# Kernel tuning notes

Hardware: AMD Instinct MI355X
Metric: run time of the kernel (lower is better)

The kernel has to match this reference:

```python
import jax, jax.numpy as jnp
import numpy as np
from jax import lax

B, N, M = 2, 16384, 4096
C1, C2 = 128, 256
H1, H2 = 256, 128  # mlp = [C1+C2, 256, 128]


def setup_inputs() -> dict:
    key = jax.random.key(0)
    ks = jax.random.split(key, 8)
    return {
        "unknown": jax.random.normal(ks[0], (B, N, 3), jnp.float32),
        "known": jax.random.normal(ks[1], (B, M, 3), jnp.float32),
        "unknow_feats": jax.random.normal(ks[2], (B, C1, N), jnp.float32),
        "known_feats": jax.random.normal(ks[3], (B, C2, M), jnp.float32),
        "W1": jax.random.normal(ks[4], (H1, C1 + C2), jnp.float32) * 0.05,
        "b1": jnp.zeros((H1,), jnp.float32),
        "W2": jax.random.normal(ks[5], (H2, H1), jnp.float32) * 0.05,
        "b2": jnp.zeros((H2,), jnp.float32),
    }


def reference(unknown, known, unknow_feats, known_feats, W1, b1, W2, b2):
    # Pairwise squared distances (B, n, m) via ||a||^2 + ||b||^2 - 2 a.b
    d2 = (
        jnp.sum(unknown * unknown, -1)[:, :, None]
        + jnp.sum(known * known, -1)[:, None, :]
        - 2.0 * jnp.einsum("bnd,bmd->bnm", unknown, known)
    )
    # 3 nearest neighbors
    neg_d2, idx = lax.top_k(-d2, 3)  # (B, n, 3)
    dist = jnp.sqrt(jnp.maximum(-neg_d2, 0.0))  # pointops returns sqrt distances
    dist_recip = 1.0 / (dist + 1e-8)
    weight = dist_recip / jnp.sum(dist_recip, axis=2, keepdims=True)  # (B, n, 3)
    # Gather neighbor features (B, C2, n, 3) and inverse-distance weighted sum
    gathered = jax.vmap(lambda f, i: f[:, i])(known_feats, idx)
    interpolated = jnp.sum(gathered * weight[:, None, :, :], axis=-1)  # (B, C2, n)
    new_features = jnp.concatenate([interpolated, unknow_feats], axis=1)  # (B, C1+C2, n)
    # Shared MLP (1x1 convs, bn=False -> conv bias + ReLU)
    h = jax.nn.relu(jnp.einsum("oc,bcn->bon", W1, new_features) + b1[None, :, None])
    out = jax.nn.relu(jnp.einsum("oc,bcn->bon", W2, h) + b2[None, :, None])
    return out  # (B, mlp[-1], n)
```

## Files before the change

kernel.cpp:

```cpp
#include <hip/hip_runtime.h>
#include <hip/hip_bf16.h>

#define BB 2
#define NN 16384
#define MM 4096
#define C1 128
#define C2 256
#define CIN 384
#define H1 256
#define H2 128
#define XROW 392
#define HROW 264
#define OS   36

typedef __attribute__((ext_vector_type(8))) short bf16x8;
typedef __attribute__((ext_vector_type(4))) float f32x4;
typedef __attribute__((ext_vector_type(2))) float f32x2;

__device__ __forceinline__ short f32_to_bf16(float x) {
    unsigned u = __float_as_uint(x);
    u += 0x7fffu + ((u >> 16) & 1u);
    return (short)(u >> 16);
}
__device__ __forceinline__ float bf16_to_f32(unsigned short u) {
    union { unsigned u; float f; } c; c.u = ((unsigned)u) << 16; return c.f;
}
__device__ __forceinline__ unsigned pack_bf16x2(float a, float b) {
    __hip_bfloat162 h = __float22bfloat162_rn(make_float2(a, b));
    union { __hip_bfloat162 h; unsigned u; } cv;
    cv.h = h;
    return cv.u;
}
__device__ __forceinline__ f32x2 score2k(f32x2 ax2, f32x2 ay2, f32x2 az2,
                                         f32x2 kx, f32x2 ky, f32x2 kz, f32x2 kn) {
    f32x2 t = __builtin_elementwise_fma(ay2, ky, kn);
    t = __builtin_elementwise_fma(ax2, kx, t);
    t = __builtin_elementwise_fma(az2, kz, t);
    return t;
}

__global__ __launch_bounds__(256) void prep_kernel(
    const float* __restrict__ KF, unsigned short* __restrict__ KT16,
    const float* __restrict__ W1, const float* __restrict__ W2,
    short* __restrict__ W1b, short* __restrict__ W2b,
    const float* __restrict__ known, float* __restrict__ kxyz)
{
    const int bx  = blockIdx.x;
    const int tid = threadIdx.x;
    if (bx < 512) {
        __shared__ short tlb[64 * 65];
        const int tb = bx >> 8;
        const int c0 = ((bx >> 6) & 3) * 64;
        const int m0 = (bx & 63) * 64;
        const int tr  = tid >> 4;
        const int tc4 = (tid & 15) * 4;
        #pragma unroll
        for (int p = 0; p < 4; ++p) {
            const int c = tr + p * 16;
            const float4 f = *(const float4*)(
                KF + ((size_t)tb * C2 + c0 + c) * MM + m0 + tc4);
            tlb[c * 65 + tc4 + 0] = f32_to_bf16(f.x);
            tlb[c * 65 + tc4 + 1] = f32_to_bf16(f.y);
            tlb[c * 65 + tc4 + 2] = f32_to_bf16(f.z);
            tlb[c * 65 + tc4 + 3] = f32_to_bf16(f.w);
        }
        __syncthreads();
        #pragma unroll
        for (int p = 0; p < 4; ++p) {
            const int m = tr + p * 16;
            ushort4 v;
            v.x = (unsigned short)tlb[(tc4 + 0) * 65 + m];
            v.y = (unsigned short)tlb[(tc4 + 1) * 65 + m];
            v.z = (unsigned short)tlb[(tc4 + 2) * 65 + m];
            v.w = (unsigned short)tlb[(tc4 + 3) * 65 + m];
            *(ushort4*)(KT16 + ((size_t)tb * MM + m0 + m) * C2 + c0 + tc4) = v;
        }
    } else if (bx < 896) {
        int i = (bx - 512) * 256 + tid;
        W1b[i] = f32_to_bf16(W1[i]);
        if (i < H2 * H1) W2b[i] = f32_to_bf16(W2[i]);
    } else {
        int i = (bx - 896) * 256 + tid;
        if (i < BB * MM) {
            float x = known[3 * i + 0], y = known[3 * i + 1], z = known[3 * i + 2];
            float n = fmaf(x, x, fmaf(y, y, z * z));
            int b = i >> 12;
            int c = i & (MM - 1);
            float* base = kxyz + (size_t)b * 16384 + (c >> 8) * 1024;
            const int pos = c & 255;
            base[pos] = x; base[256 + pos] = y; base[512 + pos] = z; base[768 + pos] = n;
        }
    }
}

__global__ __launch_bounds__(1024, 8) void fused_knn_mlp_kernel(
    const float* __restrict__ unknown,
    const float* __restrict__ kxyz,
    const float* __restrict__ unknow_feats,
    const unsigned short* __restrict__ KT16,
    const short* __restrict__ W1b, const float* __restrict__ b1,
    const short* __restrict__ W2b, const float* __restrict__ b2,
    float* __restrict__ out)
{
    __shared__ __align__(16) float candS[16384];
    __shared__ __align__(16) float red[3072];
    __shared__ float vf[64];
    __shared__ int   cnt[64];
    __shared__ int   IsL[64 * 3];
    __shared__ float WsL[64 * 3];

    const int bx    = blockIdx.x;
    const int tid   = threadIdx.x;
    const int lane  = tid & 63;
    const int w     = __builtin_amdgcn_readfirstlane(tid >> 6);
    const int b     = bx >> 8;
    const int qbase = (bx & 255) * 64;
    const int n     = qbase + lane;

    if (tid < 64) cnt[tid] = 0;

    {
        const float* kb = kxyz + (size_t)b * 16384;
        #pragma unroll
        for (int c = 0; c < 4; ++c) {
            const int i = c * 4096 + tid * 4;
            *(f32x4*)&candS[i] = *(const f32x4*)(kb + i);
        }
    }

    {
        const float ux = unknown[((size_t)b * NN + n) * 3 + 0];
        const float uy = unknown[((size_t)b * NN + n) * 3 + 1];
        const float uz = unknown[((size_t)b * NN + n) * 3 + 2];
        const f32x2 ax2 = {-2.f * ux, -2.f * ux};
        const f32x2 ay2 = {-2.f * uy, -2.f * uy};
        const f32x2 az2 = {-2.f * uz, -2.f * uz};

        const float* kw = candS + w * 1024;
        __syncthreads();

        float va0 = 3e38f, va1 = 3e38f, va2 = 3e38f;
        float vb0 = 3e38f, vb1 = 3e38f, vb2 = 3e38f;
        unsigned mlo = 0, mhi = 0;

        auto superstep = [&](int t, unsigned& mask, int bit) {
            const f32x4 X = *(const f32x4*)(kw + 4 * t);
            const f32x4 Y = *(const f32x4*)(kw + 256 + 4 * t);
            const f32x4 Z = *(const f32x4*)(kw + 512 + 4 * t);
            const f32x4 N = *(const f32x4*)(kw + 768 + 4 * t);
            const f32x2 xl = {X.x, X.y}, xh = {X.z, X.w};
            const f32x2 yl = {Y.x, Y.y}, yh = {Y.z, Y.w};
            const f32x2 zl = {Z.x, Z.y}, zh = {Z.z, Z.w};
            const f32x2 nl = {N.x, N.y}, nh = {N.z, N.w};
            const f32x2 sl = score2k(ax2, ay2, az2, xl, yl, zl, nl);
            const f32x2 sh = score2k(ax2, ay2, az2, xh, yh, zh, nh);
            const float thr = fmaxf(va2, vb2);
            const float pm  = fminf(fminf(fminf(sl.x, sl.y), sh.x), sh.y);
            mask |= (pm <= thr) ? (1u << bit) : 0u;
            va2 = __builtin_amdgcn_fmed3f(va1, sl.x, va2);
            va1 = __builtin_amdgcn_fmed3f(va0, sl.x, va1);
            va0 = fminf(sl.x, va0);
            vb2 = __builtin_amdgcn_fmed3f(vb1, sl.y, vb2);
            vb1 = __builtin_amdgcn_fmed3f(vb0, sl.y, vb1);
            vb0 = fminf(sl.y, vb0);
            va2 = __builtin_amdgcn_fmed3f(va1, sh.x, va2);
            va1 = __builtin_amdgcn_fmed3f(va0, sh.x, va1);
            va0 = fminf(sh.x, va0);
            vb2 = __builtin_amdgcn_fmed3f(vb1, sh.y, vb2);
            vb1 = __builtin_amdgcn_fmed3f(vb0, sh.y, vb1);
            vb0 = fminf(sh.y, vb0);
        };
        #pragma unroll 2
        for (int t = 0; t < 32; ++t) superstep(t, mlo, t);
        #pragma unroll 2
        for (int t = 32; t < 64; ++t) superstep(t, mhi, t - 32);

        {
            float bv[3] = {vb0, vb1, vb2};
            #pragma unroll
            for (int k = 0; k < 3; ++k) {
                float d = bv[k];
                va2 = __builtin_amdgcn_fmed3f(va1, d, va2);
                va1 = __builtin_amdgcn_fmed3f(va0, d, va1);
                va0 = fminf(d, va0);
            }
        }
        red[(w * 64 + lane) * 3 + 0] = va0;
        red[(w * 64 + lane) * 3 + 1] = va1;
        red[(w * 64 + lane) * 3 + 2] = va2;
        __syncthreads();

        if (tid < 64) {
            float r0 = 3e38f, r1 = 3e38f, r2 = 3e38f;
            #pragma unroll
            for (int ww = 0; ww < 16; ++ww) {
                #pragma unroll
                for (int k = 0; k < 3; ++k) {
                    float d = red[(ww * 64 + tid) * 3 + k];
                    r2 = __builtin_amdgcn_fmed3f(r1, d, r2);
                    r1 = __builtin_amdgcn_fmed3f(r0, d, r1);
                    r0 = fminf(d, r0);
                }
            }
            vf[tid] = r2;
        }
        __syncthreads();

        float* mscp = red;
        int*   midp = (int*)red + 512;
        const float v2f = vf[lane];
        auto rescan = [&](int tt) {
            const f32x4 X = *(const f32x4*)(kw + 4 * tt);
            const f32x4 Y = *(const f32x4*)(kw + 256 + 4 * tt);
            const f32x4 Z = *(const f32x4*)(kw + 512 + 4 * tt);
            const f32x4 N = *(const f32x4*)(kw + 768 + 4 * tt);
            const f32x2 xl = {X.x, X.y}, xh = {X.z, X.w};
            const f32x2 yl = {Y.x, Y.y}, yh = {Y.z, Y.w};
            const f32x2 zl = {Z.x, Z.y}, zh = {Z.z, Z.w};
            const f32x2 nl = {N.x, N.y}, nh = {N.z, N.w};
            const f32x2 sl = score2k(ax2, ay2, az2, xl, yl, zl, nl);
            const f32x2 sh = score2k(ax2, ay2, az2, xh, yh, zh, nh);
            const float sv[4] = {sl.x, sl.y, sh.x, sh.y};
            #pragma unroll
            for (int j = 0; j < 4; ++j) {
                if (sv[j] <= v2f) {
                    int slot = atomicAdd(&cnt[lane], 1);
                    if (slot < 8) {
                        mscp[lane * 8 + slot] = sv[j];
                        midp[lane * 8 + slot] = w * 256 + 4 * tt + j;
                    }
                }
            }
        };
        unsigned m = mlo;
        while (m) { int t = __builtin_ctz(m); m &= m - 1; rescan(t); }
        m = mhi;
        while (m) { int t = __builtin_ctz(m); m &= m - 1; rescan(t + 32); }
        __syncthreads();

        if (tid < 64) {
            const int c = cnt[tid] < 8 ? cnt[tid] : 8;
            float r0 = 3e38f, r1 = 3e38f, r2 = 3e38f;
            int   q0 = 0x7FFFFFFF, q1 = 0x7FFFFFFF, q2 = 0x7FFFFFFF;
            #pragma unroll
            for (int k = 0; k < 8; ++k) {
                float d = (k < c) ? mscp[tid * 8 + k] : 3e38f;
                int   j = (k < c) ? midp[tid * 8 + k] : 0x7FFFFFFF;
                const bool lt0 = (d < r0) || (d == r0 && j < q0);
                const bool lt1 = (d < r1) || (d == r1 && j < q1);
                const bool lt2 = (d < r2) || (d == r2 && j < q2);
                float nr2 = lt1 ? r1 : (lt2 ? d : r2);
                int   nq2 = lt1 ? q1 : (lt2 ? j : q2);
                float nr1 = lt0 ? r0 : (lt1 ? d : r1);
                int   nq1 = lt0 ? q0 : (lt1 ? j : q1);
                float nr0 = lt0 ? d : r0;
                int   nq0 = lt0 ? j : q0;
                r0 = nr0; r1 = nr1; r2 = nr2; q0 = nq0; q1 = nq1; q2 = nq2;
            }
            const float* up = unknown + ((size_t)b * NN + qbase + tid) * 3;
            const float uxx = up[0], uyy = up[1], uzz = up[2];
            const float unq = fmaf(uxx, uxx, fmaf(uyy, uyy, uzz * uzz));
            float d0 = sqrtf(fmaxf(r0 + unq, 0.f));
            float d1 = sqrtf(fmaxf(r1 + unq, 0.f));
            float d2 = sqrtf(fmaxf(r2 + unq, 0.f));
            float i0 = 1.f / (d0 + 1e-8f);
            float i1 = 1.f / (d1 + 1e-8f);
            float i2 = 1.f / (d2 + 1e-8f);
            float s  = i0 + i1 + i2;
            IsL[tid * 3 + 0] = q0; IsL[tid * 3 + 1] = q1; IsL[tid * 3 + 2] = q2;
            WsL[tid * 3 + 0] = i0 / s; WsL[tid * 3 + 1] = i1 / s; WsL[tid * 3 + 2] = i2 / s;
        }
    }
    __syncthreads();

    const unsigned short* KTb = KT16 + (size_t)b * MM * C2;
    short* XH_s = (short*)candS;
    short* Hs_s = (short*)candS + 32 * XROW;
    float* outS = candS;
    const int lr = lane & 15;
    const int lq = lane >> 4;
    const int c4 = lane << 2;

    for (int tile = 0; tile < 2; ++tile) {
        const int pbase = tile * 32;

        {
            ushort4 g[2][3];
            #pragma unroll
            for (int j = 0; j < 2; ++j) {
                const int pi = (pbase + 2 * w + j) * 3;
                g[j][0] = *(const ushort4*)(KTb + (size_t)IsL[pi + 0] * C2 + c4);
                g[j][1] = *(const ushort4*)(KTb + (size_t)IsL[pi + 1] * C2 + c4);
                g[j][2] = *(const ushort4*)(KTb + (size_t)IsL[pi + 2] * C2 + c4);
            }
            #pragma unroll
            for (int j = 0; j < 2; ++j) {
                const int pl = 2 * w + j;
                const int pi = (pbase + pl) * 3;
                const float w0 = WsL[pi + 0], w1 = WsL[pi + 1], w2 = WsL[pi + 2];
                float vx = fmaf(w0, bf16_to_f32(g[j][0].x), fmaf(w1, bf16_to_f32(g[j][1].x), w2 * bf16_to_f32(g[j][2].x)));
                float vy = fmaf(w0, bf16_to_f32(g[j][0].y), fmaf(w1, bf16_to_f32(g[j][1].y), w2 * bf16_to_f32(g[j][2].y)));
                float vz = fmaf(w0, bf16_to_f32(g[j][0].z), fmaf(w1, bf16_to_f32(g[j][1].z), w2 * bf16_to_f32(g[j][2].z)));
                float vw = fmaf(w0, bf16_to_f32(g[j][0].w), fmaf(w1, bf16_to_f32(g[j][1].w), w2 * bf16_to_f32(g[j][2].w)));
                uint2 pk;
                pk.x = pack_bf16x2(vx, vy);
                pk.y = pack_bf16x2(vz, vw);
                *(uint2*)&XH_s[pl * XROW + c4] = pk;
            }
            const float* UFb = unknow_feats + (size_t)b * C1 * NN + qbase + pbase;
            const int cc = tid >> 3;
            const int nq = (tid & 7) << 2;
            const float4 f = *(const float4*)(UFb + (size_t)cc * NN + nq);
            XH_s[(nq + 0) * XROW + C2 + cc] = f32_to_bf16(f.x);
            XH_s[(nq + 1) * XROW + C2 + cc] = f32_to_bf16(f.y);
            XH_s[(nq + 2) * XROW + C2 + cc] = f32_to_bf16(f.z);
            XH_s[(nq + 3) * XROW + C2 + cc] = f32_to_bf16(f.w);
        }
        __syncthreads();

        f32x4 acc1[2];
        acc1[0] = (f32x4){0.f, 0.f, 0.f, 0.f};
        acc1[1] = (f32x4){0.f, 0.f, 0.f, 0.f};
        #pragma unroll 4
        for (int k0 = 0; k0 < CIN; k0 += 32) {
            bf16x8 a  = *(const bf16x8*)(W1b + (size_t)(w * 16 + lr) * CIN + k0 + lq * 8);
            bf16x8 x0 = *(bf16x8*)&XH_s[lr * XROW + k0 + lq * 8];
            bf16x8 x1 = *(bf16x8*)&XH_s[(16 + lr) * XROW + k0 + lq * 8];
            acc1[0] = __builtin_amdgcn_mfma_f32_16x16x32_bf16(a, x0, acc1[0], 0, 0, 0);
            acc1[1] = __builtin_amdgcn_mfma_f32_16x16x32_bf16(a, x1, acc1[1], 0, 0, 0);
        }
        {
            const int ob = w * 16 + lq * 4;
            float bb0 = b1[ob + 0], bb1 = b1[ob + 1], bb2 = b1[ob + 2], bb3 = b1[ob + 3];
            #pragma unroll
            for (int p = 0; p < 2; ++p) {
                uint2 pk;
                pk.x = pack_bf16x2(fmaxf(acc1[p].x + bb0, 0.f),
                                   fmaxf(acc1[p].y + bb1, 0.f));
                pk.y = pack_bf16x2(fmaxf(acc1[p].z + bb2, 0.f),
                                   fmaxf(acc1[p].w + bb3, 0.f));
                *(uint2*)&Hs_s[(p * 16 + lr) * HROW + ob] = pk;
            }
        }
        __syncthreads();

        {
            const int r0 = (w & 7) * 16;
            const int pg = (w >> 3) * 16;
            f32x4 acc2 = (f32x4){0.f, 0.f, 0.f, 0.f};
            #pragma unroll 4
            for (int k0 = 0; k0 < H1; k0 += 32) {
                bf16x8 a2 = *(const bf16x8*)(W2b + (size_t)(r0 + lr) * H1 + k0 + lq * 8);
                bf16x8 h  = *(bf16x8*)&Hs_s[(pg + lr) * HROW + k0 + lq * 8];
                acc2 = __builtin_amdgcn_mfma_f32_16x16x32_bf16(a2, h, acc2, 0, 0, 0);
            }
            #pragma unroll
            for (int r = 0; r < 4; ++r) {
                const int o = r0 + lq * 4 + r;
                outS[o * OS + pg + lr] =
                    fmaxf(((const float*)&acc2)[r] + b2[o], 0.f);
            }
        }
        __syncthreads();

        {
            const int o = tid >> 3;
            const int k = (tid & 7) << 2;
            const f32x4 v = *(const f32x4*)&outS[o * OS + k];
            *(f32x4*)(out + ((size_t)b * H2 + o) * NN + qbase + pbase + k) = v;
        }
        __syncthreads();
    }
}

extern "C" void kernel_launch(void* const* d_in, const int* in_sizes, int n_in,
                              void* d_out, int out_size, void* d_ws, size_t ws_size,
                              hipStream_t stream) {
    const float* unknown      = (const float*)d_in[0];
    const float* known        = (const float*)d_in[1];
    const float* unknow_feats = (const float*)d_in[2];
    const float* known_feats  = (const float*)d_in[3];
    const float* W1           = (const float*)d_in[4];
    const float* b1           = (const float*)d_in[5];
    const float* W2           = (const float*)d_in[6];
    const float* b2           = (const float*)d_in[7];
    float* out = (float*)d_out;

    char* ws = (char*)d_ws;
    short*          W1b  = (short*)(ws);
    short*          W2b  = (short*)(ws + 196608);
    float*          kxyz = (float*)(ws + 262144);
    unsigned short* KT16 = (unsigned short*)(ws + 393216);

    prep_kernel<<<928, 256, 0, stream>>>(
        known_feats, KT16, W1, W2, W1b, W2b, known, kxyz);

    fused_knn_mlp_kernel<<<512, 1024, 0, stream>>>(
        unknown, kxyz, unknow_feats, KT16, W1b, b1, W2b, b2, out);
}
```

Before: 157.2 us.

## Move weight bf16 conversion and known-point SoA prep into fused kernel

Removes the weight-conversion and known-xyz repacking work from the prep kernel. The fused kernel now reads raw fp32 W1/W2 and converts them to bf16 in registers before each MFMA. It also loads the raw known xyz, scatters it into the SoA shared-memory layout and computes the norms in place. The aim is a lighter prep kernel with fewer workspace round-trips, at the cost of redundant per-block conversion, twice the global weight bytes in the MLP loops, and an extra barrier.

Result: slower. 194.4 us (+23.7%).

```diff
diff --git a/kernel.cpp b/kernel.cpp
--- a/kernel.cpp
+++ b/kernel.cpp
@@ -40,66 +40,46 @@
 }
 
 __global__ __launch_bounds__(256) void prep_kernel(
-    const float* __restrict__ KF, unsigned short* __restrict__ KT16,
-    const float* __restrict__ W1, const float* __restrict__ W2,
-    short* __restrict__ W1b, short* __restrict__ W2b,
-    const float* __restrict__ known, float* __restrict__ kxyz)
+    const float* __restrict__ KF, unsigned short* __restrict__ KT16)
 {
+    __shared__ short tlb[64 * 65];
     const int bx  = blockIdx.x;
     const int tid = threadIdx.x;
-    if (bx < 512) {
-        __shared__ short tlb[64 * 65];
-        const int tb = bx >> 8;
-        const int c0 = ((bx >> 6) & 3) * 64;
-        const int m0 = (bx & 63) * 64;
-        const int tr  = tid >> 4;
-        const int tc4 = (tid & 15) * 4;
-        #pragma unroll
-        for (int p = 0; p < 4; ++p) {
-            const int c = tr + p * 16;
-            const float4 f = *(const float4*)(
-                KF + ((size_t)tb * C2 + c0 + c) * MM + m0 + tc4);
-            tlb[c * 65 + tc4 + 0] = f32_to_bf16(f.x);
-            tlb[c * 65 + tc4 + 1] = f32_to_bf16(f.y);
-            tlb[c * 65 + tc4 + 2] = f32_to_bf16(f.z);
-            tlb[c * 65 + tc4 + 3] = f32_to_bf16(f.w);
-        }
-        __syncthreads();
-        #pragma unroll
-        for (int p = 0; p < 4; ++p) {
-            const int m = tr + p * 16;
-            ushort4 v;
-            v.x = (unsigned short)tlb[(tc4 + 0) * 65 + m];
-            v.y = (unsigned short)tlb[(tc4 + 1) * 65 + m];
-            v.z = (unsigned short)tlb[(tc4 + 2) * 65 + m];
-            v.w = (unsigned short)tlb[(tc4 + 3) * 65 + m];
-            *(ushort4*)(KT16 + ((size_t)tb * MM + m0 + m) * C2 + c0 + tc4) = v;
-        }
-    } else if (bx < 896) {
-        int i = (bx - 512) * 256 + tid;
-        W1b[i] = f32_to_bf16(W1[i]);
-        if (i < H2 * H1) W2b[i] = f32_to_bf16(W2[i]);
-    } else {
-        int i = (bx - 896) * 256 + tid;
-        if (i < BB * MM) {
-            float x = known[3 * i + 0], y = known[3 * i + 1], z = known[3 * i + 2];
-            float n = fmaf(x, x, fmaf(y, y, z * z));
-            int b = i >> 12;
-            int c = i & (MM - 1);
-            float* base = kxyz + (size_t)b * 16384 + (c >> 8) * 1024;
-            const int pos = c & 255;
-            base[pos] = x; base[256 + pos] = y; base[512 + pos] = z; base[768 + pos] = n;
-        }
+    const int tb = bx >> 8;
+    const int c0 = ((bx >> 6) & 3) * 64;
+    const int m0 = (bx & 63) * 64;
+    const int tr  = tid >> 4;
+    const int tc4 = (tid & 15) * 4;
+    #pragma unroll
+    for (int p = 0; p < 4; ++p) {
+        const int c = tr + p * 16;
+        const float4 f = *(const float4*)(
+            KF + ((size_t)tb * C2 + c0 + c) * MM + m0 + tc4);
+        tlb[c * 65 + tc4 + 0] = f32_to_bf16(f.x);
+        tlb[c * 65 + tc4 + 1] = f32_to_bf16(f.y);
+        tlb[c * 65 + tc4 + 2] = f32_to_bf16(f.z);
+        tlb[c * 65 + tc4 + 3] = f32_to_bf16(f.w);
+    }
+    __syncthreads();
+    #pragma unroll
+    for (int p = 0; p < 4; ++p) {
+        const int m = tr + p * 16;
+        ushort4 v;
+        v.x = (unsigned short)tlb[(tc4 + 0) * 65 + m];
+        v.y = (unsigned short)tlb[(tc4 + 1) * 65 + m];
+        v.z = (unsigned short)tlb[(tc4 + 2) * 65 + m];
+        v.w = (unsigned short)tlb[(tc4 + 3) * 65 + m];
+        *(ushort4*)(KT16 + ((size_t)tb * MM + m0 + m) * C2 + c0 + tc4) = v;
     }
 }
 
 __global__ __launch_bounds__(1024, 8) void fused_knn_mlp_kernel(
     const float* __restrict__ unknown,
-    const float* __restrict__ kxyz,
+    const float* __restrict__ known,
     const float* __restrict__ unknow_feats,
     const unsigned short* __restrict__ KT16,
-    const short* __restrict__ W1b, const float* __restrict__ b1,
-    const short* __restrict__ W2b, const float* __restrict__ b2,
+    const float* __restrict__ W1, const float* __restrict__ b1,
+    const float* __restrict__ W2, const float* __restrict__ b2,
     float* __restrict__ out)
 {
     __shared__ __align__(16) float candS[16384];
@@ -120,12 +100,30 @@
     if (tid < 64) cnt[tid] = 0;
 
     {
-        const float* kb = kxyz + (size_t)b * 16384;
+        const float* kb0 = known + (size_t)b * MM * 3;
         #pragma unroll
-        for (int c = 0; c < 4; ++c) {
-            const int i = c * 4096 + tid * 4;
-            *(f32x4*)&candS[i] = *(const f32x4*)(kb + i);
-        }
+        for (int k = 0; k < 3; ++k) {
+            const int i = (k * 1024 + tid) * 4;
+            const f32x4 f = *(const f32x4*)(kb0 + i);
+            #pragma unroll
+            for (int j = 0; j < 4; ++j) {
+                const unsigned fi = i + j;
+                const unsigned p  = fi / 3u;
+                const unsigned cc = fi - 3u * p;
+                candS[(p >> 8) * 1024 + cc * 256 + (p & 255)] =
+                    ((const float*)&f)[j];
+            }
+        }
+        __syncthreads();
+        const int ci  = tid * 4;
+        float* base = candS + (ci >> 8) * 1024;
+        const int pos = ci & 255;
+        const f32x4 X = *(const f32x4*)&base[pos];
+        const f32x4 Y = *(const f32x4*)&base[256 + pos];
+        const f32x4 Z = *(const f32x4*)&base[512 + pos];
+        const f32x4 Nv = __builtin_elementwise_fma(X, X,
+                         __builtin_elementwise_fma(Y, Y, Z * Z));
+        *(f32x4*)&base[768 + pos] = Nv;
     }
 
     {
@@ -323,11 +321,18 @@
         acc1[1] = (f32x4){0.f, 0.f, 0.f, 0.f};
         #pragma unroll 4
         for (int k0 = 0; k0 < CIN; k0 += 32) {
-            bf16x8 a  = *(const bf16x8*)(W1b + (size_t)(w * 16 + lr) * CIN + k0 + lq * 8);
+            const float* wp = W1 + (size_t)(w * 16 + lr) * CIN + k0 + lq * 8;
+            const f32x4 wA = *(const f32x4*)wp;
+            const f32x4 wB = *(const f32x4*)(wp + 4);
+            union { unsigned u[4]; bf16x8 v; } aw;
+            aw.u[0] = pack_bf16x2(wA.x, wA.y);
+            aw.u[1] = pack_bf16x2(wA.z, wA.w);
+            aw.u[2] = pack_bf16x2(wB.x, wB.y);
+            aw.u[3] = pack_bf16x2(wB.z, wB.w);
             bf16x8 x0 = *(bf16x8*)&XH_s[lr * XROW + k0 + lq * 8];
             bf16x8 x1 = *(bf16x8*)&XH_s[(16 + lr) * XROW + k0 + lq * 8];
-            acc1[0] = __builtin_amdgcn_mfma_f32_16x16x32_bf16(a, x0, acc1[0], 0, 0, 0);
-            acc1[1] = __builtin_amdgcn_mfma_f32_16x16x32_bf16(a, x1, acc1[1], 0, 0, 0);
+            acc1[0] = __builtin_amdgcn_mfma_f32_16x16x32_bf16(aw.v, x0, acc1[0], 0, 0, 0);
+            acc1[1] = __builtin_amdgcn_mfma_f32_16x16x32_bf16(aw.v, x1, acc1[1], 0, 0, 0);
         }
         {
             const int ob = w * 16 + lq * 4;
@@ -350,9 +355,16 @@
             f32x4 acc2 = (f32x4){0.f, 0.f, 0.f, 0.f};
             #pragma unroll 4
             for (int k0 = 0; k0 < H1; k0 += 32) {
-                bf16x8 a2 = *(const bf16x8*)(W2b + (size_t)(r0 + lr) * H1 + k0 + lq * 8);
-                bf16x8 h  = *(bf16x8*)&Hs_s[(pg + lr) * HROW + k0 + lq * 8];
-                acc2 = __builtin_amdgcn_mfma_f32_16x16x32_bf16(a2, h, acc2, 0, 0, 0);
+                const float* wp = W2 + (size_t)(r0 + lr) * H1 + k0 + lq * 8;
+                const f32x4 wA = *(const f32x4*)wp;
+                const f32x4 wB = *(const f32x4*)(wp + 4);
+                union { unsigned u[4]; bf16x8 v; } aw;
+                aw.u[0] = pack_bf16x2(wA.x, wA.y);
+                aw.u[1] = pack_bf16x2(wA.z, wA.w);
+                aw.u[2] = pack_bf16x2(wB.x, wB.y);
+                aw.u[3] = pack_bf16x2(wB.z, wB.w);
+                bf16x8 h = *(bf16x8*)&Hs_s[(pg + lr) * HROW + k0 + lq * 8];
+                acc2 = __builtin_amdgcn_mfma_f32_16x16x32_bf16(aw.v, h, acc2, 0, 0, 0);
             }
             #pragma unroll
             for (int r = 0; r < 4; ++r) {
@@ -386,15 +398,10 @@
     const float* b2           = (const float*)d_in[7];
     float* out = (float*)d_out;
 
-    char* ws = (char*)d_ws;
-    short*          W1b  = (short*)(ws);
-    short*          W2b  = (short*)(ws + 196608);
-    float*          kxyz = (float*)(ws + 262144);
-    unsigned short* KT16 = (unsigned short*)(ws + 393216);
-
-    prep_kernel<<<928, 256, 0, stream>>>(
-        known_feats, KT16, W1, W2, W1b, W2b, known, kxyz);
+    unsigned short* KT16 = (unsigned short*)d_ws;
+
+    prep_kernel<<<512, 256, 0, stream>>>(known_feats, KT16);
 
     fused_knn_mlp_kernel<<<512, 1024, 0, stream>>>(
-        unknown, kxyz, unknow_feats, KT16, W1b, b1, W2b, b2, out);
-}
+        unknown, known, unknow_feats, KT16, W1, b1, W2, b2, out);
+}
```
